# Optimization experiments

Hardware: AMD Instinct MI355X
Metric: run time of the kernel (lower is better)

## Reference

```python
import jax, jax.numpy as jnp
import numpy as np

C, H, N, B, L = 1, 512, 64, 16, 2048  # n_channels, n_heads, d_kernel, batch, seq_len


def setup_inputs() -> dict:
    key = jax.random.key(0)
    k1, k2 = jax.random.split(key)
    u = jax.random.normal(k1, (B, C * H, L), dtype=jnp.float32)
    k = jax.random.normal(k2, (C, H, N), dtype=jnp.float32)
    return {"u": u, "k": k}


def _l1_normalize(x, axis):
    # torch.linalg.norm(x, ord=1, dim=axis, keepdim=True): vector 1-norm along `axis`
    return x / jnp.sum(jnp.abs(x), axis=axis, keepdims=True)


def _forward(u, k):
    c, h, n = k.shape
    bsz, d, l = u.shape  # d == c*h
    dt = u.dtype
    # Shift matrix A: A[:, :, 1:, :-1] = I  (companion-style shift)
    A = jnp.zeros((c, h, n, n), dtype=dt).at[:, :, 1:, :-1].set(jnp.eye(n - 1, dtype=dt))
    # b = e1 broadcast to (c, h, n)
    b_vec = jnp.zeros((c, h, n), dtype=dt).at[:, :, 0].set(1.0)
    # closed-loop: k_norm = L1-normalize(clamp(k, 1/16, 1)); A_cl = L1-normalize(A + b k^T)
    k_norm = _l1_normalize(jnp.clip(k, 1.0 / 16.0, 1.0), axis=2)
    BK = jnp.einsum('chi,chj->chij', b_vec, k_norm)
    M = _l1_normalize(A + BK, axis=2)

    # Krylov recurrence: f[i] = k . (M^i b), i = 0..l-1
    def step(x, _):
        f_i = jnp.einsum('chn,chn->ch', k, x)
        x_next = jnp.einsum('chij,chj->chi', M, x)
        return x_next, f_i

    _, f = jax.lax.scan(step, b_vec, None, length=l)  # f: (l, c, h)
    f = jnp.moveaxis(f, 0, -1)  # (c, h, l)

    # Causal FFT convolution of u (b, c, h, l) with filter f (c, h, l)
    n_fft = 2 * l
    uf = jnp.fft.rfft(u.reshape(bsz, c, h, l), n=n_fft)
    ff = jnp.fft.rfft(f, n=n_fft)
    y = jnp.fft.irfft(uf * ff[None], n=n_fft)[..., :l]
    return y.reshape(bsz, c * h, l)


def reference(u, k):
    return _forward(u, k)
```

## Files before the change

### kernel.cpp

```cpp
#include <hip/hip_runtime.h>


namespace {

constexpr int kH = 512;
constexpr int kL = 2048;

typedef __attribute__((ext_vector_type(8))) short bf16x8;
typedef __attribute__((ext_vector_type(4))) float f32x4;

#define MFMA(A, B, C) __builtin_amdgcn_mfma_f32_16x16x32_bf16((A), (B), (C), 0, 0, 0)

__device__ inline unsigned int cvt_pk_bf16(float lo, float hi) {
  unsigned int r;
  asm("v_cvt_pk_bf16_f32 %0, %1, %2" : "=v"(r) : "v"(lo), "v"(hi));
  return r;
}

union B8U4 { bf16x8 v; unsigned int u[4]; };

__device__ inline void cvt_split8(const f32x4 a, const f32x4 b, bf16x8& fh, bf16x8& fl) {
  B8U4 H, L;
  float x[8];
  #pragma unroll
  for (int j = 0; j < 4; ++j) { x[j] = a[j]; x[4 + j] = b[j]; }
  #pragma unroll
  for (int d = 0; d < 4; ++d) {
    const float x0 = x[2 * d], x1 = x[2 * d + 1];
    const unsigned int hp = cvt_pk_bf16(x0, x1);
    const float h0 = __uint_as_float(hp << 16);
    const float h1 = __uint_as_float(hp & 0xFFFF0000u);
    H.u[d] = hp;
    L.u[d] = cvt_pk_bf16(x0 - h0, x1 - h1);
  }
  fh = H.v; fl = L.v;
}

__device__ inline void gen_frag(const float* tp, int n0, bf16x8& fh, bf16x8& fl) {
  float t[8];
  #pragma unroll
  for (int j = 0; j < 8; ++j) {
    const int n = n0 - j;
    t[j] = (n >= 0 && n < 127) ? tp[n] : 0.0f;
  }
  const f32x4 a = {t[0], t[1], t[2], t[3]};
  const f32x4 b = {t[4], t[5], t[6], t[7]};
  cvt_split8(a, b, fh, fl);
}

__device__ inline void gen_fragB(const float* tp, int base, bf16x8& fh, bf16x8& fl) {
  float t[8];
  #pragma unroll
  for (int j = 0; j < 8; ++j) t[j] = tp[base + j];
  const f32x4 a = {t[0], t[1], t[2], t[3]};
  const f32x4 b = {t[4], t[5], t[6], t[7]};
  cvt_split8(a, b, fh, fl);
}


__global__ __launch_bounds__(256, 1)
void ssm_mfma_kernel(const float* __restrict__ u,
                     const float* __restrict__ kin,
                     float* __restrict__ y) {
  const int h    = blockIdx.x;
  const int tid  = threadIdx.x;
  const int wid  = tid >> 6;
  const int lane = tid & 63;
  const int ln16 = lane & 15;
  const int quad = lane >> 4;

  __shared__ alignas(16) char pool[123136];
  auto cring   = (float (*)[4][16][68]) (pool);
  auto Astage  = (float (*)[68]) (pool);
  auto Pstage  = (float (*)[68]) (pool + 17408);
  auto pring   = (bf16x8 (*)[4][4][64]) (pool + 34816);
  auto S_T     = (bf16x8 (*)[2][2][64]) (pool + 67584);
  auto G2S_T   = (bf16x8 (*)[2][2][64]) (pool + 83968);
  auto Gp_T    = (bf16x8 (*)[2][2][64]) (pool + 100352);
  auto scratch = (float (*)[68]) (pool + 116736);
  auto taps    = (float (*)[128]) (pool + 121088);
  float* wPad  = (float*) (pool + 122624);

  if (wid == 0) {
    const float kv = kin[h * 64 + lane];
    const float kc = fminf(fmaxf(kv, 0.0625f), 1.0f);
    float ks = kc;
    #pragma unroll
    for (int off = 32; off >= 1; off >>= 1) ks += __shfl_xor(ks, off);
    const float kn = kc / ks;
    const float cc = 1.0f / (1.0f + kn);
    float pp = cc;
    #pragma unroll
    for (int off = 1; off < 64; off <<= 1) {
      const float t = __shfl_up(pp, off);
      if (lane >= off) pp *= t;
    }
    float Pe = __shfl_up(pp, 1);
    if (lane == 0) Pe = 1.0f;
    const float wv = (lane < 63) ? (kn * cc * Pe) : Pe;
    const float gv = kv * Pe;
    float sv = (lane == 0) ? 1.0f : 0.0f;
    for (int rr = 0; rr < 63; ++rr) {
      const float s0 = __shfl(sv, rr);
      const float cf = __shfl(wv, lane - 1 - rr);
      if (lane > rr) sv = fmaf(cf, s0, sv);
    }
    taps[0][lane] = 0.0f;
    taps[1][lane] = 0.0f;
    const float gn = __shfl(gv, lane + 1);
    taps[2][lane] = (lane < 63) ? gn : 0.0f;
    taps[2][64 + lane] = 0.0f;
    taps[0][63 + lane] = sv;
    taps[1][63 + lane] = gv;
    if (lane == 0) { taps[0][127] = 0.0f; taps[1][127] = 0.0f; }
    wPad[lane] = wv;
    wPad[64 + lane] = 0.0f;
  }
  __syncthreads();

  {
    const int mt = wid;
    bf16x8 xh[2], xl[2], g2h[2], g2l[2];
    #pragma unroll
    for (int tk = 0; tk < 2; ++tk) {
      const int n0 = 16 * mt + ln16 - (32 * tk + 8 * quad) + 63;
      gen_frag(taps[0], n0, xh[tk], xl[tk]);
      gen_frag(taps[1], n0, g2h[tk], g2l[tk]);
    }
    #pragma unroll
    for (int nt = 0; nt < 4; ++nt) {
      f32x4 accA = {0.f, 0.f, 0.f, 0.f};
      f32x4 accG = {0.f, 0.f, 0.f, 0.f};
      #pragma unroll
      for (int tk = 0; tk < 2; ++tk) {
        const int base = 8 * quad + 32 * tk - (16 * nt + ln16) + 63;
        bf16x8 bh, bl;
        gen_fragB(wPad, base, bh, bl);
        accA = MFMA(xh[tk], bh, accA);
        accA = MFMA(xh[tk], bl, accA);
        accA = MFMA(xl[tk], bh, accA);
        accA = MFMA(xl[tk], bl, accA);
        bf16x8 sbh, sbl;
        gen_fragB(taps[0], base, sbh, sbl);
        accG = MFMA(g2h[tk], sbh, accG);
        accG = MFMA(g2h[tk], sbl, accG);
        accG = MFMA(g2l[tk], sbh, accG);
      }
      #pragma unroll
      for (int r = 0; r < 4; ++r) {
        Astage[16 * mt + 4 * quad + r][16 * nt + ln16] = accA[r];
        Pstage[16 * mt + 4 * quad + r][16 * nt + ln16] = accG[r];
      }
    }
  }
  __syncthreads();

  {
    const int mt = wid;
    #pragma unroll
    for (int tk = 0; tk < 2; ++tk) {
      const int n0 = 16 * mt + ln16 - (32 * tk + 8 * quad) + 63;
      bf16x8 fh, fl;
      gen_frag(taps[0], n0, fh, fl);
      S_T[mt][tk][0][lane] = fh;  S_T[mt][tk][1][lane] = fl;
      const int row = 16 * mt + ln16, k0 = 32 * tk + 8 * quad;
      const f32x4 a = *(const f32x4*)&Pstage[row][k0];
      const f32x4 b = *(const f32x4*)&Pstage[row][k0 + 4];
      cvt_split8(a, b, fh, fl);
      G2S_T[mt][tk][0][lane] = fh;  G2S_T[mt][tk][1][lane] = fl;
    }
  }
  __syncthreads();

  {
    const int mt = wid;
    bf16x8 g2h[2], g2l[2];
    #pragma unroll
    for (int tk = 0; tk < 2; ++tk) {
      const int n0 = 16 * mt + ln16 - (32 * tk + 8 * quad) + 63;
      gen_frag(taps[1], n0, g2h[tk], g2l[tk]);
    }
    #pragma unroll
    for (int nt = 0; nt < 4; ++nt) {
      f32x4 acc = {0.f, 0.f, 0.f, 0.f};
      #pragma unroll
      for (int tk = 0; tk < 2; ++tk) {
        float t[8];
        #pragma unroll
        for (int j = 0; j < 8; ++j)
          t[j] = Astage[8 * quad + 32 * tk + j][16 * nt + ln16];
        const f32x4 a = {t[0], t[1], t[2], t[3]};
        const f32x4 b = {t[4], t[5], t[6], t[7]};
        bf16x8 bh, bl;
        cvt_split8(a, b, bh, bl);
        acc = MFMA(g2h[tk], bh, acc);
        acc = MFMA(g2h[tk], bl, acc);
        acc = MFMA(g2l[tk], bh, acc);
      }
      #pragma unroll
      for (int r = 0; r < 4; ++r) {
        const int i = 16 * mt + 4 * quad + r, j = 16 * nt + ln16;
        Pstage[i][j] = acc[r] + taps[2][(i - j) + 63];
      }
    }
  }
  __syncthreads();

  bf16x8 aH[4][2], aL[4][2];
  {
    const int mt = wid;
    #pragma unroll
    for (int tk = 0; tk < 2; ++tk) {
      const int row = 16 * mt + ln16, k0 = 32 * tk + 8 * quad;
      const f32x4 a = *(const f32x4*)&Pstage[row][k0];
      const f32x4 b = *(const f32x4*)&Pstage[row][k0 + 4];
      bf16x8 fh, fl;
      cvt_split8(a, b, fh, fl);
      Gp_T[mt][tk][0][lane] = fh;  Gp_T[mt][tk][1][lane] = fl;
    }
  }
  if (wid == 0) {
    #pragma unroll
    for (int mt = 0; mt < 4; ++mt) {
      #pragma unroll
      for (int tk = 0; tk < 2; ++tk) {
        const int row = 16 * mt + ln16, k0 = 32 * tk + 8 * quad;
        const f32x4 a = *(const f32x4*)&Astage[row][k0];
        const f32x4 b = *(const f32x4*)&Astage[row][k0 + 4];
        cvt_split8(a, b, aH[mt][tk], aL[mt][tk]);
      }
    }
  }
  __syncthreads();

  bf16x8 pH[2], pL[2];
  {
    bf16x8 z;
    #pragma unroll
    for (int j = 0; j < 8; ++j) z[j] = 0;
    pH[0] = z; pH[1] = z; pL[0] = z; pL[1] = z;
  }

  const float* ub = u + ((size_t)ln16 * kH + h) * kL + 8 * quad;
  float* yb = y + ((size_t)ln16 * kH + h) * kL;

  f32x4 urC[4][4];
  if (wid != 0) {
    #pragma unroll
    for (int cj = 0; cj < 4; ++cj)
      #pragma unroll
      for (int i = 0; i < 4; ++i)
        urC[cj][i] = *(const f32x4*)(ub + 64 * cj + 32 * (i >> 1) + 4 * (i & 1));
  }

  f32x4 yuE[6], yuO[6];

  auto step = [&](int s, f32x4 (&yu)[6]) {
    if (wid == 0) {
      if (s >= 1 && s <= 8) {
        const int g = s - 1, gp = g & 1;
        for (int cj = 0; cj < 4; ++cj) {
          pring[gp][cj][0][lane] = pH[0];
          pring[gp][cj][1][lane] = pH[1];
          pring[gp][cj][2][lane] = pL[0];
          pring[gp][cj][3][lane] = pL[1];
          #pragma unroll
          for (int mt = 0; mt < 4; ++mt) {
            f32x4 acc = *(const f32x4*)&cring[gp][cj][ln16][16 * mt + 4 * quad];
            #pragma unroll
            for (int tk = 0; tk < 2; ++tk) {
              acc = MFMA(aH[mt][tk], pH[tk], acc);
              acc = MFMA(aH[mt][tk], pL[tk], acc);
              acc = MFMA(aL[mt][tk], pH[tk], acc);
            }
            *(f32x4*)&scratch[ln16][16 * mt + 4 * quad] = acc;
          }
          asm volatile("s_waitcnt lgkmcnt(0)" ::: "memory");
          __builtin_amdgcn_sched_barrier(0);
          #pragma unroll
          for (int tk = 0; tk < 2; ++tk) {
            const int k0 = 8 * quad + 32 * tk;
            const f32x4 ra = *(const f32x4*)&scratch[ln16][k0];
            const f32x4 rb = *(const f32x4*)&scratch[ln16][k0 + 4];
            cvt_split8(ra, rb, pH[tk], pL[tk]);
          }
        }
      }
    } else {
      bf16x8 uH[4][2], uL[4][2];
      if (s < 8) {
        #pragma unroll
        for (int cj = 0; cj < 4; ++cj) {
          cvt_split8(urC[cj][0], urC[cj][1], uH[cj][0], uL[cj][0]);
          cvt_split8(urC[cj][2], urC[cj][3], uH[cj][1], uL[cj][1]);
        }
        if (s < 7) {
          #pragma unroll
          for (int cj = 0; cj < 4; ++cj)
            #pragma unroll
            for (int i = 0; i < 4; ++i)
              urC[cj][i] = *(const f32x4*)(ub + 64 * (4 * (s + 1) + cj) +
                                           32 * (i >> 1) + 4 * (i & 1));
        }
      }
      if (s >= 2) {
        const int gf = s - 2;
        #pragma unroll
        for (int cj = 0; cj < 4; ++cj) {
          bf16x8 pfH[2], pfL[2];
          pfH[0] = pring[s & 1][cj][0][lane];
          pfH[1] = pring[s & 1][cj][1][lane];
          pfL[0] = pring[s & 1][cj][2][lane];
          pfL[1] = pring[s & 1][cj][3][lane];
          #pragma unroll
          for (int mt = 0; mt < 4; ++mt) {
            const int t = 4 * cj + mt, li = t / 3;
            if ((t % 3) + 1 == wid) {
              f32x4 acc = yu[li];
              #pragma unroll
              for (int tk = 0; tk < 2; ++tk) {
                const bf16x8 gh = Gp_T[mt][tk][0][lane];
                const bf16x8 gl = Gp_T[mt][tk][1][lane];
                acc = MFMA(gh, pfH[tk], acc);
                acc = MFMA(gh, pfL[tk], acc);
                acc = MFMA(gl, pfH[tk], acc);
              }
              *(f32x4*)(yb + 64 * (4 * gf + cj) + 16 * mt + 4 * quad) = acc;
            }
          }
        }
      }
      if (s < 8) {
        #pragma unroll
        for (int cj = 0; cj < 4; ++cj) {
          #pragma unroll
          for (int mt = 0; mt < 4; ++mt) {
            const int t = 4 * cj + mt, li = t / 3;
            if ((t % 3) + 1 == wid) {
              f32x4 accC = {0.f, 0.f, 0.f, 0.f};
              f32x4 accU = {0.f, 0.f, 0.f, 0.f};
              #pragma unroll
              for (int tk = 0; tk < 2; ++tk) {
                const bf16x8 sh = S_T[mt][tk][0][lane];
                const bf16x8 sl = S_T[mt][tk][1][lane];
                accC = MFMA(sh, uH[cj][tk], accC);
                accC = MFMA(sh, uL[cj][tk], accC);
                accC = MFMA(sl, uH[cj][tk], accC);
                const bf16x8 gh = G2S_T[mt][tk][0][lane];
                const bf16x8 gl = G2S_T[mt][tk][1][lane];
                accU = MFMA(gh, uH[cj][tk], accU);
                accU = MFMA(gh, uL[cj][tk], accU);
                accU = MFMA(gl, uH[cj][tk], accU);
              }
              *(f32x4*)&cring[s & 1][cj][ln16][16 * mt + 4 * quad] = accC;
              yu[li] = accU;
            }
          }
        }
      }
    }
    asm volatile("s_waitcnt lgkmcnt(0)" ::: "memory");
    __builtin_amdgcn_s_barrier();
    asm volatile("" ::: "memory");
  };

  #pragma unroll 1
  for (int sb = 0; sb < 5; ++sb) {
    step(2 * sb,     yuE);
    step(2 * sb + 1, yuO);
  }
}

}

extern "C" void kernel_launch(void* const* d_in, const int* in_sizes, int n_in,
                              void* d_out, int out_size, void* d_ws, size_t ws_size,
                              hipStream_t stream) {
  const float* u  = (const float*)d_in[0];
  const float* kk = (const float*)d_in[1];
  if (n_in >= 2 && in_sizes[0] < in_sizes[1]) {
    const float* t = u; u = kk; kk = t;
  }
  float* yy = (float*)d_out;
  hipLaunchKernelGGL(ssm_mfma_kernel, dim3(kH), dim3(256), 0, stream, u, kk, yy);
}
```

Before: 173.9 us.

## Restructure chunk pipeline: 5 waves, one 64-wide chunk per step, smaller LDS

The chunked recurrence pipeline now processes one 64-sample chunk per barrier step instead of four, with 32 steps. It uses 320 threads where four consumer waves each own one 16-row tile, and the S matrix fragments are held in registers instead of LDS. LDS drops from about 123KB to about 70KB and launch bounds allow 3 blocks per CU, to raise occupancy and overlap across heads. The trade-off is many more barriers and a shorter serial chain per step on wave 0, which may expose more latency.

```diff
diff --git a/kernel.cpp b/kernel.cpp
--- a/kernel.cpp
+++ b/kernel.cpp
@@ -5,6 +5,7 @@
 
 constexpr int kH = 512;
 constexpr int kL = 2048;
+constexpr int kChunks = 32;
 
 typedef __attribute__((ext_vector_type(8))) short bf16x8;
 typedef __attribute__((ext_vector_type(4))) float f32x4;
@@ -58,7 +59,7 @@
 }
 
 
-__global__ __launch_bounds__(256, 1)
+__global__ __launch_bounds__(320, 3)
 void ssm_mfma_kernel(const float* __restrict__ u,
                      const float* __restrict__ kin,
                      float* __restrict__ y) {
@@ -69,17 +70,16 @@
   const int ln16 = lane & 15;
   const int quad = lane >> 4;
 
-  __shared__ alignas(16) char pool[123136];
-  auto cring   = (float (*)[4][16][68]) (pool);
+  __shared__ alignas(16) char pool[69632];
   auto Astage  = (float (*)[68]) (pool);
   auto Pstage  = (float (*)[68]) (pool + 17408);
-  auto pring   = (bf16x8 (*)[4][4][64]) (pool + 34816);
-  auto S_T     = (bf16x8 (*)[2][2][64]) (pool + 67584);
-  auto G2S_T   = (bf16x8 (*)[2][2][64]) (pool + 83968);
-  auto Gp_T    = (bf16x8 (*)[2][2][64]) (pool + 100352);
-  auto scratch = (float (*)[68]) (pool + 116736);
-  auto taps    = (float (*)[128]) (pool + 121088);
-  float* wPad  = (float*) (pool + 122624);
+  auto cring   = (float (*)[16][68]) (pool);
+  auto scratch = (float (*)[68]) (pool + 8704);
+  auto pring   = (bf16x8 (*)[4][64]) (pool + 17408);
+  auto G2S_T   = (bf16x8 (*)[2][2][64]) (pool + 34816);
+  auto Gp_T    = (bf16x8 (*)[2][2][64]) (pool + 51200);
+  auto taps    = (float (*)[128]) (pool + 67584);
+  float* wPad  = (float*) (pool + 69120);
 
   if (wid == 0) {
     const float kv = kin[h * 64 + lane];
@@ -118,7 +118,7 @@
   }
   __syncthreads();
 
-  {
+  if (wid < 4) {
     const int mt = wid;
     bf16x8 xh[2], xl[2], g2h[2], g2l[2];
     #pragma unroll
@@ -155,24 +155,30 @@
   }
   __syncthreads();
 
-  {
-    const int mt = wid;
-    #pragma unroll
-    for (int tk = 0; tk < 2; ++tk) {
-      const int n0 = 16 * mt + ln16 - (32 * tk + 8 * quad) + 63;
-      bf16x8 fh, fl;
-      gen_frag(taps[0], n0, fh, fl);
-      S_T[mt][tk][0][lane] = fh;  S_T[mt][tk][1][lane] = fl;
-      const int row = 16 * mt + ln16, k0 = 32 * tk + 8 * quad;
+  const int cmt = (wid >= 1) ? (wid - 1) : 0;
+  bf16x8 sH[2], sL[2];
+  if (wid >= 1) {
+    #pragma unroll
+    for (int tk = 0; tk < 2; ++tk) {
+      const int n0 = 16 * cmt + ln16 - (32 * tk + 8 * quad) + 63;
+      gen_frag(taps[0], n0, sH[tk], sL[tk]);
+    }
+  }
+  if (wid < 4) {
+    #pragma unroll
+    for (int tk = 0; tk < 2; ++tk) {
+      const int row = 16 * wid + ln16, k0 = 32 * tk + 8 * quad;
       const f32x4 a = *(const f32x4*)&Pstage[row][k0];
       const f32x4 b = *(const f32x4*)&Pstage[row][k0 + 4];
+      bf16x8 fh, fl;
       cvt_split8(a, b, fh, fl);
-      G2S_T[mt][tk][0][lane] = fh;  G2S_T[mt][tk][1][lane] = fl;
-    }
-  }
-  __syncthreads();
-
-  {
+      G2S_T[wid][tk][0][lane] = fh;
+      G2S_T[wid][tk][1][lane] = fl;
+    }
+  }
+  __syncthreads();
+
+  if (wid < 4) {
     const int mt = wid;
     bf16x8 g2h[2], g2l[2];
     #pragma unroll
@@ -207,16 +213,16 @@
   __syncthreads();
 
   bf16x8 aH[4][2], aL[4][2];
-  {
-    const int mt = wid;
-    #pragma unroll
-    for (int tk = 0; tk < 2; ++tk) {
-      const int row = 16 * mt + ln16, k0 = 32 * tk + 8 * quad;
+  if (wid < 4) {
+    #pragma unroll
+    for (int tk = 0; tk < 2; ++tk) {
+      const int row = 16 * wid + ln16, k0 = 32 * tk + 8 * quad;
       const f32x4 a = *(const f32x4*)&Pstage[row][k0];
       const f32x4 b = *(const f32x4*)&Pstage[row][k0 + 4];
       bf16x8 fh, fl;
       cvt_split8(a, b, fh, fl);
-      Gp_T[mt][tk][0][lane] = fh;  Gp_T[mt][tk][1][lane] = fl;
+      Gp_T[wid][tk][0][lane] = fh;
+      Gp_T[wid][tk][1][lane] = fl;
     }
   }
   if (wid == 0) {
@@ -244,120 +250,91 @@
   const float* ub = u + ((size_t)ln16 * kH + h) * kL + 8 * quad;
   float* yb = y + ((size_t)ln16 * kH + h) * kL;
 
-  f32x4 urC[4][4];
-  if (wid != 0) {
-    #pragma unroll
-    for (int cj = 0; cj < 4; ++cj)
-      #pragma unroll
-      for (int i = 0; i < 4; ++i)
-        urC[cj][i] = *(const f32x4*)(ub + 64 * cj + 32 * (i >> 1) + 4 * (i & 1));
-  }
-
-  f32x4 yuE[6], yuO[6];
-
-  auto step = [&](int s, f32x4 (&yu)[6]) {
+  f32x4 uv[4];
+  if (wid >= 1) {
+    #pragma unroll
+    for (int i = 0; i < 4; ++i)
+      uv[i] = *(const f32x4*)(ub + 32 * (i >> 1) + 4 * (i & 1));
+  }
+  f32x4 yuA = {0.f, 0.f, 0.f, 0.f}, yuB = {0.f, 0.f, 0.f, 0.f};
+
+  auto step = [&](int s, f32x4& yu) {
     if (wid == 0) {
-      if (s >= 1 && s <= 8) {
-        const int g = s - 1, gp = g & 1;
-        for (int cj = 0; cj < 4; ++cj) {
-          pring[gp][cj][0][lane] = pH[0];
-          pring[gp][cj][1][lane] = pH[1];
-          pring[gp][cj][2][lane] = pL[0];
-          pring[gp][cj][3][lane] = pL[1];
-          #pragma unroll
-          for (int mt = 0; mt < 4; ++mt) {
-            f32x4 acc = *(const f32x4*)&cring[gp][cj][ln16][16 * mt + 4 * quad];
-            #pragma unroll
-            for (int tk = 0; tk < 2; ++tk) {
-              acc = MFMA(aH[mt][tk], pH[tk], acc);
-              acc = MFMA(aH[mt][tk], pL[tk], acc);
-              acc = MFMA(aL[mt][tk], pH[tk], acc);
-            }
-            *(f32x4*)&scratch[ln16][16 * mt + 4 * quad] = acc;
-          }
-          asm volatile("s_waitcnt lgkmcnt(0)" ::: "memory");
-          __builtin_amdgcn_sched_barrier(0);
+      if (s >= 1 && s <= kChunks) {
+        const int par = (s - 1) & 1;
+        pring[par][0][lane] = pH[0];
+        pring[par][1][lane] = pH[1];
+        pring[par][2][lane] = pL[0];
+        pring[par][3][lane] = pL[1];
+        f32x4 acc[4];
+        #pragma unroll
+        for (int mt = 0; mt < 4; ++mt)
+          acc[mt] = *(const f32x4*)&cring[par][ln16][16 * mt + 4 * quad];
+        #pragma unroll
+        for (int mt = 0; mt < 4; ++mt) {
           #pragma unroll
           for (int tk = 0; tk < 2; ++tk) {
-            const int k0 = 8 * quad + 32 * tk;
-            const f32x4 ra = *(const f32x4*)&scratch[ln16][k0];
-            const f32x4 rb = *(const f32x4*)&scratch[ln16][k0 + 4];
-            cvt_split8(ra, rb, pH[tk], pL[tk]);
+            acc[mt] = MFMA(aH[mt][tk], pH[tk], acc[mt]);
+            acc[mt] = MFMA(aH[mt][tk], pL[tk], acc[mt]);
+            acc[mt] = MFMA(aL[mt][tk], pH[tk], acc[mt]);
           }
+          *(f32x4*)&scratch[ln16][16 * mt + 4 * quad] = acc[mt];
+        }
+        asm volatile("s_waitcnt lgkmcnt(0)" ::: "memory");
+        __builtin_amdgcn_sched_barrier(0);
+        #pragma unroll
+        for (int tk = 0; tk < 2; ++tk) {
+          const int k0 = 8 * quad + 32 * tk;
+          const f32x4 ra = *(const f32x4*)&scratch[ln16][k0];
+          const f32x4 rb = *(const f32x4*)&scratch[ln16][k0 + 4];
+          cvt_split8(ra, rb, pH[tk], pL[tk]);
         }
       }
     } else {
-      bf16x8 uH[4][2], uL[4][2];
-      if (s < 8) {
-        #pragma unroll
-        for (int cj = 0; cj < 4; ++cj) {
-          cvt_split8(urC[cj][0], urC[cj][1], uH[cj][0], uL[cj][0]);
-          cvt_split8(urC[cj][2], urC[cj][3], uH[cj][1], uL[cj][1]);
-        }
-        if (s < 7) {
-          #pragma unroll
-          for (int cj = 0; cj < 4; ++cj)
-            #pragma unroll
-            for (int i = 0; i < 4; ++i)
-              urC[cj][i] = *(const f32x4*)(ub + 64 * (4 * (s + 1) + cj) +
-                                           32 * (i >> 1) + 4 * (i & 1));
+      f32x4 accU = {0.f, 0.f, 0.f, 0.f};
+      if (s < kChunks) {
+        bf16x8 uH[2], uL[2];
+        cvt_split8(uv[0], uv[1], uH[0], uL[0]);
+        cvt_split8(uv[2], uv[3], uH[1], uL[1]);
+        const int tn = (s + 1 < kChunks) ? 64 * (s + 1) : 0;
+        #pragma unroll
+        for (int i = 0; i < 4; ++i)
+          uv[i] = *(const f32x4*)(ub + tn + 32 * (i >> 1) + 4 * (i & 1));
+        f32x4 accC = {0.f, 0.f, 0.f, 0.f};
+        #pragma unroll
+        for (int tk = 0; tk < 2; ++tk) {
+          accC = MFMA(sH[tk], uH[tk], accC);
+          accC = MFMA(sH[tk], uL[tk], accC);
+          accC = MFMA(sL[tk], uH[tk], accC);
+        }
+        *(f32x4*)&cring[s & 1][ln16][16 * cmt + 4 * quad] = accC;
+        #pragma unroll
+        for (int tk = 0; tk < 2; ++tk) {
+          const bf16x8 gh = G2S_T[cmt][tk][0][lane];
+          const bf16x8 gl = G2S_T[cmt][tk][1][lane];
+          accU = MFMA(gh, uH[tk], accU);
+          accU = MFMA(gh, uL[tk], accU);
+          accU = MFMA(gl, uH[tk], accU);
         }
       }
       if (s >= 2) {
-        const int gf = s - 2;
-        #pragma unroll
-        for (int cj = 0; cj < 4; ++cj) {
-          bf16x8 pfH[2], pfL[2];
-          pfH[0] = pring[s & 1][cj][0][lane];
-          pfH[1] = pring[s & 1][cj][1][lane];
-          pfL[0] = pring[s & 1][cj][2][lane];
-          pfL[1] = pring[s & 1][cj][3][lane];
-          #pragma unroll
-          for (int mt = 0; mt < 4; ++mt) {
-            const int t = 4 * cj + mt, li = t / 3;
-            if ((t % 3) + 1 == wid) {
-              f32x4 acc = yu[li];
-              #pragma unroll
-              for (int tk = 0; tk < 2; ++tk) {
-                const bf16x8 gh = Gp_T[mt][tk][0][lane];
-                const bf16x8 gl = Gp_T[mt][tk][1][lane];
-                acc = MFMA(gh, pfH[tk], acc);
-                acc = MFMA(gh, pfL[tk], acc);
-                acc = MFMA(gl, pfH[tk], acc);
-              }
-              *(f32x4*)(yb + 64 * (4 * gf + cj) + 16 * mt + 4 * quad) = acc;
-            }
-          }
-        }
-      }
-      if (s < 8) {
-        #pragma unroll
-        for (int cj = 0; cj < 4; ++cj) {
-          #pragma unroll
-          for (int mt = 0; mt < 4; ++mt) {
-            const int t = 4 * cj + mt, li = t / 3;
-            if ((t % 3) + 1 == wid) {
-              f32x4 accC = {0.f, 0.f, 0.f, 0.f};
-              f32x4 accU = {0.f, 0.f, 0.f, 0.f};
-              #pragma unroll
-              for (int tk = 0; tk < 2; ++tk) {
-                const bf16x8 sh = S_T[mt][tk][0][lane];
-                const bf16x8 sl = S_T[mt][tk][1][lane];
-                accC = MFMA(sh, uH[cj][tk], accC);
-                accC = MFMA(sh, uL[cj][tk], accC);
-                accC = MFMA(sl, uH[cj][tk], accC);
-                const bf16x8 gh = G2S_T[mt][tk][0][lane];
-                const bf16x8 gl = G2S_T[mt][tk][1][lane];
-                accU = MFMA(gh, uH[cj][tk], accU);
-                accU = MFMA(gh, uL[cj][tk], accU);
-                accU = MFMA(gl, uH[cj][tk], accU);
-              }
-              *(f32x4*)&cring[s & 1][cj][ln16][16 * mt + 4 * quad] = accC;
-              yu[li] = accU;
-            }
-          }
-        }
-      }
+        bf16x8 pfH[2], pfL[2];
+        pfH[0] = pring[s & 1][0][lane];
+        pfH[1] = pring[s & 1][1][lane];
+        pfL[0] = pring[s & 1][2][lane];
+        pfL[1] = pring[s & 1][3][lane];
+        f32x4 accY = yu;
+        #pragma unroll
+        for (int tk = 0; tk < 2; ++tk) {
+          const bf16x8 gh = Gp_T[cmt][tk][0][lane];
+          const bf16x8 gl = Gp_T[cmt][tk][1][lane];
+          accY = MFMA(gh, pfH[tk], accY);
+          accY = MFMA(gh, pfL[tk], accY);
+          accY = MFMA(gl, pfH[tk], accY);
+        }
+        *(f32x4*)(yb + 64 * (s - 2) + 16 * cmt + 4 * quad) = accY;
+      }
+      yu = accU;
     }
     asm volatile("s_waitcnt lgkmcnt(0)" ::: "memory");
     __builtin_amdgcn_s_barrier();
@@ -365,9 +342,9 @@
   };
 
   #pragma unroll 1
-  for (int sb = 0; sb < 5; ++sb) {
-    step(2 * sb,     yuE);
-    step(2 * sb + 1, yuO);
+  for (int i = 0; i < 17; ++i) {
+    step(2 * i,     yuA);
+    step(2 * i + 1, yuB);
   }
 }
 
@@ -382,5 +359,5 @@
     const float* t = u; u = kk; kk = t;
   }
   float* yy = (float*)d_out;
-  hipLaunchKernelGGL(ssm_mfma_kernel, dim3(kH), dim3(256), 0, stream, u, kk, yy);
-}
+  hipLaunchKernelGGL(ssm_mfma_kernel, dim3(kH), dim3(320), 0, stream, u, kk, yy);
+}
```

After: 192.4 us. 1.11x slower.
